# Kernel optimization log

Hardware: AMD Instinct MI355X
Metric: run time of the kernel (lower is better)

Reference implementation:

```python
import jax, jax.numpy as jnp
import numpy as np

H_IMG, W_IMG = 256, 256
FX = FY = 300.0
CX, CY = W_IMG / 2.0, H_IMG / 2.0
NEAR, FAR = 0.01, 100.0
MAX_RADIUS = 64.0
N_GAUSS = 4096


def quat_to_rot(q):
    q = q / jnp.linalg.norm(q, axis=-1, keepdims=True)
    w, x, y, z = q[..., 0], q[..., 1], q[..., 2], q[..., 3]
    R = jnp.stack([
        1 - 2 * y * y - 2 * z * z, 2 * x * y - 2 * w * z, 2 * x * z + 2 * w * y,
        2 * x * y + 2 * w * z, 1 - 2 * x * x - 2 * z * z, 2 * y * z - 2 * w * x,
        2 * x * z - 2 * w * y, 2 * y * z + 2 * w * x, 1 - 2 * x * x - 2 * y * y,
    ], axis=-1)
    return R.reshape(q.shape[:-1] + (3, 3))


def setup_inputs():
    key = jax.random.key(0)
    k1, k2, k3, k4, k5, k6 = jax.random.split(key, 6)
    xy = jax.random.normal(k1, (N_GAUSS, 2), jnp.float32) * 2.0
    z = -(jax.random.uniform(k2, (N_GAUSS, 1), jnp.float32) * 6.0 + 2.0)  # depths in [2, 8]
    positions = jnp.concatenate([xy, z], axis=1)
    scales = jax.random.uniform(k3, (N_GAUSS, 3), jnp.float32) * 0.10 + 0.02
    rotations = jax.random.normal(k4, (N_GAUSS, 4), jnp.float32)
    colors = jax.random.uniform(k5, (N_GAUSS, 3), jnp.float32)
    opacities = jax.random.uniform(k6, (N_GAUSS,), jnp.float32) * 0.8 + 0.1
    view_matrix = jnp.eye(4, dtype=jnp.float32)
    return {"positions": positions, "scales": scales, "rotations": rotations,
            "colors": colors, "opacities": opacities, "view_matrix": view_matrix}


def _render(positions, scales, rotations, colors, opacities, view_matrix):
    N = positions.shape[0]
    pts = jnp.concatenate([positions, jnp.ones((N, 1), positions.dtype)], axis=1)
    pc = (view_matrix @ pts.T).T[:, :3]  # camera-space points (N,3)
    x, y, z = pc[:, 0], pc[:, 1], pc[:, 2]
    depths = -z
    z_safe = jnp.clip(jnp.abs(z), 0.01) * jnp.sign(z + 1e-8)
    z2 = z_safe * z_safe
    # 3D covariance = (Rcam R S)(Rcam R S)^T
    R = quat_to_rot(rotations)
    R_cam = view_matrix[:3, :3] @ R
    RS = R_cam * scales[:, None, :]  # right-multiply by diag(scales)
    cov3d = RS @ jnp.swapaxes(RS, -1, -2)
    # perspective Jacobian (N,2,3)
    zr = jnp.zeros_like(x)
    J = jnp.stack([
        jnp.stack([FX / -z_safe, zr, FX * x / z2], axis=-1),
        jnp.stack([zr, FY / z_safe, FY * y / z2], axis=-1),
    ], axis=-2)
    cov2d = J @ cov3d @ jnp.swapaxes(J, -1, -2)
    u = FX * x / -z_safe + CX
    v = FY * -y / -z_safe + CY
    # effective radius: 3 sigma from max eigenvalue of 2x2 covariance
    a, b = cov2d[:, 0, 0], cov2d[:, 0, 1]
    c, d = cov2d[:, 1, 0], cov2d[:, 1, 1]
    tr = a + d
    det = jnp.clip(a * d - b * c, 1e-6)
    disc = jnp.clip(tr * tr - 4.0 * det, 0.0)
    lam = (tr + jnp.sqrt(disc)) * 0.5
    radii = jnp.minimum(3.0 * jnp.sqrt(jnp.clip(lam, 1e-6)), MAX_RADIUS)
    # depth sort (front to back)
    order = jnp.argsort(depths)
    u, v, a, b, c, d = u[order], v[order], a[order], b[order], c[order], d[order]
    radii, depths = radii[order], depths[order]
    colors_s, op_s = colors[order], opacities[order]
    # visibility culling: zero opacity instead of compaction (same math, static shapes)
    visible = (depths > NEAR) & (depths < FAR)
    visible &= (u + radii > 0) & (u - radii < W_IMG)
    visible &= (v + radii > 0) & (v - radii < H_IMG)
    op_s = jnp.where(visible, op_s, 0.0)
    # regularized 2x2 inverse (pinv of PD matrix == inverse)
    ar, dr = a + 1e-4, d + 1e-4
    inv_det = 1.0 / (ar * dr - b * c)
    ia, ib, ic, idd = dr * inv_det, -b * inv_det, -c * inv_det, ar * inv_det
    px = jnp.arange(W_IMG, dtype=jnp.float32)[None, :]
    py = jnp.arange(H_IMG, dtype=jnp.float32)[:, None]

    def step(carry, g):
        acc_c, acc_a = carry
        mx, my, gia, gib, gic, gid, r, col, o = g
        dx = px - mx  # (1,W)
        dy = py - my  # (H,1)
        power = -0.5 * (gia * dx * dx + (gib + gic) * dx * dy + gid * dy * dy)
        # bounding-box mask replicating the torch tile bounds [int(m-r), int(m+r)+1)
        inside = ((px >= jnp.trunc(mx - r)) & (px <= jnp.trunc(mx + r))
                  & (py >= jnp.trunc(my - r)) & (py <= jnp.trunc(my + r)))
        alpha = jnp.where(inside, o * jnp.exp(power), 0.0)
        w = alpha * (1.0 - acc_a)  # front-to-back over-compositing
        return (acc_c + w[..., None] * col, acc_a + w), None

    acc0 = (jnp.zeros((H_IMG, W_IMG, 3), jnp.float32),
            jnp.zeros((H_IMG, W_IMG), jnp.float32))
    (acc_c, acc_a), _ = jax.lax.scan(
        step, acc0, (u, v, ia, ib, ic, idd, radii, colors_s, op_s))
    bg = jnp.zeros(3, jnp.float32)
    img = acc_c + (1.0 - acc_a)[..., None] * bg
    return jnp.transpose(img, (2, 0, 1))  # (3,H,W)


def reference(positions, scales, rotations, colors, opacities, view_matrix):
    return _render(positions, scales, rotations, colors, opacities, view_matrix)
```

## Files before the change

### kernel.cpp

```cpp
#include <hip/hip_runtime.h>
#include <hip/hip_fp16.h>
#include <math.h>

#define N_G   4096
#define CAP   1024
#define W_IMG 256
#define H_IMG 256

__global__ __launch_bounds__(256) void prep(
    const float* __restrict__ pos, const float* __restrict__ scl,
    const float* __restrict__ rot, const float* __restrict__ col,
    const float* __restrict__ opa, const float* __restrict__ vm,
    float4* __restrict__ gaussU, short4* __restrict__ bbhU,
    float* __restrict__ depthU)
{
  const int i = blockIdx.x * 256 + threadIdx.x;
  if (i >= N_G) return;
  const float FX=300.f, FY=300.f, CXc=128.f, CYc=128.f;
  const float HLOG2E = 0.72134752f;
  float V00=vm[0],V01=vm[1],V02=vm[2],V03=vm[3];
  float V10=vm[4],V11=vm[5],V12=vm[6],V13=vm[7];
  float V20=vm[8],V21=vm[9],V22=vm[10],V23=vm[11];
  float p0=pos[3*i], p1=pos[3*i+1], p2=pos[3*i+2];
  float X = V00*p0+V01*p1+V02*p2+V03;
  float Y = V10*p0+V11*p1+V12*p2+V13;
  float Z = V20*p0+V21*p1+V22*p2+V23;
  float depth = -Z;
  float zp = Z + 1e-8f;
  float sgn = (zp>0.f)?1.f:((zp<0.f)?-1.f:0.f);
  float z_safe = fmaxf(fabsf(Z), 0.01f) * sgn;
  float z2 = z_safe*z_safe;
  float qw=rot[4*i], qx=rot[4*i+1], qy=rot[4*i+2], qz=rot[4*i+3];
  float qi = 1.f/sqrtf(qw*qw+qx*qx+qy*qy+qz*qz);
  qw*=qi; qx*=qi; qy*=qi; qz*=qi;
  float R00=1.f-2.f*qy*qy-2.f*qz*qz, R01=2.f*qx*qy-2.f*qw*qz, R02=2.f*qx*qz+2.f*qw*qy;
  float R10=2.f*qx*qy+2.f*qw*qz, R11=1.f-2.f*qx*qx-2.f*qz*qz, R12=2.f*qy*qz-2.f*qw*qx;
  float R20=2.f*qx*qz-2.f*qw*qy, R21=2.f*qy*qz+2.f*qw*qx, R22=1.f-2.f*qx*qx-2.f*qy*qy;
  float C00=V00*R00+V01*R10+V02*R20, C01=V00*R01+V01*R11+V02*R21, C02=V00*R02+V01*R12+V02*R22;
  float C10=V10*R00+V11*R10+V12*R20, C11=V10*R01+V11*R11+V12*R21, C12=V10*R02+V11*R12+V12*R22;
  float C20=V20*R00+V21*R10+V22*R20, C21=V20*R01+V21*R11+V22*R21, C22=V20*R02+V21*R12+V22*R22;
  float s0=scl[3*i], s1=scl[3*i+1], s2=scl[3*i+2];
  float S00=C00*s0,S01=C01*s1,S02=C02*s2;
  float S10=C10*s0,S11=C11*s1,S12=C12*s2;
  float S20=C20*s0,S21=C21*s1,S22=C22*s2;
  float c00=S00*S00+S01*S01+S02*S02;
  float c01=S00*S10+S01*S11+S02*S12;
  float c02=S00*S20+S01*S21+S02*S22;
  float c11=S10*S10+S11*S11+S12*S12;
  float c12=S10*S20+S11*S21+S12*S22;
  float c22=S20*S20+S21*S21+S22*S22;
  float j00=FX/(-z_safe), j02=FX*X/z2;
  float j11=FY/z_safe,    j12=FY*Y/z2;
  float M00=j00*c00+j02*c02, M01=j00*c01+j02*c12, M02=j00*c02+j02*c22;
  float M10=j11*c01+j12*c02, M11=j11*c11+j12*c12, M12=j11*c12+j12*c22;
  float a =M00*j00+M02*j02;
  float b =M01*j11+M02*j12;
  float c_=M10*j00+M12*j02;
  float d =M11*j11+M12*j12;
  float u = FX*X/(-z_safe)+CXc;
  float v = FY*(-Y)/(-z_safe)+CYc;
  float tr=a+d;
  float det=fmaxf(a*d-b*c_, 1e-6f);
  float disc=fmaxf(tr*tr-4.f*det, 0.f);
  float lam=(tr+sqrtf(disc))*0.5f;
  float radius=fminf(3.f*sqrtf(fmaxf(lam,1e-6f)), 64.f);
  bool vis = (depth>0.01f)&&(depth<100.f)
          && (u+radius>0.f)&&(u-radius<(float)W_IMG)
          && (v+radius>0.f)&&(v-radius<(float)H_IMG);
  float o = vis ? opa[i] : 0.f;
  float ar=a+1e-4f, dr=d+1e-4f;
  float inv=1.f/(ar*dr-b*c_);
  short4 bb = make_short4(1000, -1000, 1000, -1000);
  if (o>0.f) {
    bb.x=(short)truncf(u-radius); bb.y=(short)truncf(u+radius);
    bb.z=(short)truncf(v-radius); bb.w=(short)truncf(v+radius);
  }
  unsigned hrg = (unsigned)__half_as_ushort(__float2half_rn(col[3*i]))
               | ((unsigned)__half_as_ushort(__float2half_rn(col[3*i+1]))<<16);
  depthU[i] = depth;
  bbhU[i]   = bb;
  gaussU[2*i]   = make_float4(u, v, (dr*inv)*HLOG2E,
                              ((-b*inv)+(-c_*inv))*HLOG2E);
  gaussU[2*i+1] = make_float4((ar*inv)*HLOG2E, log2f(o),
                              __uint_as_float(hrg), col[3*i+2]);
}

__global__ __launch_bounds__(1024) void render(
    const short4* __restrict__ bbhU, const float4* __restrict__ gaussU,
    const float* __restrict__ depthU, float* __restrict__ out)
{
  __shared__ __align__(16) unsigned long long keys[CAP+2];
  __shared__ unsigned short sidx[CAP];
  __shared__ float4 gp[CAP*2];
  __shared__ short4 bbh[CAP];
  __shared__ float4 res[16][64];
  __shared__ unsigned long long smsk[64];
  __shared__ int scnt[64], soff[64], slen;

  const int tid = threadIdx.x, wv = tid>>6, lane = tid&63;
  const int bid = (int)((blockIdx.x * 331u) & 511u);
  const int RX0=(bid&15)*16, RY0=(bid>>4)*8;
  const int RX1=RX0+15, RY1=RY0+7;

  {
    short4 bb[4];
    #pragma unroll
    for (int c4=0;c4<4;c4++) bb[c4]=bbhU[(wv*4+c4)*64+lane];
    #pragma unroll
    for (int c4=0;c4<4;c4++) {
      int c=wv*4+c4;
      bool pred=(bb[c4].y>=RX0)&&(bb[c4].x<=RX1)&&(bb[c4].w>=RY0)&&(bb[c4].z<=RY1);
      unsigned long long m=__ballot(pred);
      if(lane==0){ smsk[c]=m; scnt[c]=__popcll(m); }
    }
  }
  __syncthreads();
  if (wv==0) {
    int cc=scnt[lane];
    int x=cc;
    #pragma unroll
    for(int d=1;d<64;d<<=1){ int y=__shfl_up(x,d); if(lane>=d) x+=y; }
    soff[lane]=x-cc;
    if(lane==63) slen=(x<CAP)?x:CAP;
  }
  __syncthreads();
  const int len=slen;
  #pragma unroll
  for (int c4=0;c4<4;c4++) {
    int c=wv*4+c4;
    unsigned long long m=smsk[c];
    int off=soff[c];
    if((m>>lane)&1ull){
      int p=off+__popcll(m&((1ull<<lane)-1ull));
      int idx=c*64+lane;
      if(p<CAP)
        keys[p]=((unsigned long long)__float_as_uint(depthU[idx])<<12)
               |(unsigned)idx;
    }
  }
  if(tid==0){ keys[len]=~0ull; keys[len+1]=~0ull; }
  __syncthreads();

  if(tid<len){
    unsigned long long kj=keys[tid];
    int r=0;
    const ulonglong2* k2=(const ulonglong2*)keys;
    int n2=(len+1)>>1;
    for(int s2=0;s2<n2;s2++){
      ulonglong2 kv=k2[s2];
      r += (kv.x<kj)+(kv.y<kj);
    }
    sidx[r]=(unsigned short)(kj&4095u);
  }
  __syncthreads();
  if(tid<len){
    int idx=(int)sidx[tid];
    gp[2*tid]  =gaussU[2*idx];
    gp[2*tid+1]=gaussU[2*idx+1];
    bbh[tid]   =bbhU[idx];
  }
  __syncthreads();

  const int t=wv>>3, seg=wv&7;
  const int TX0=RX0+t*8, TY0=RY0, TX1=TX0+7, TY1=TY0+7;
  const int ipx=TX0+(lane&7), ipy=TY0+(lane>>3);
  const float px=(float)ipx, py=(float)ipy;
  const int segLen=(len+7)>>3;
  const int s=seg*segLen;
  int e=s+segLen; if(e>len) e=len;
  float aR=0.f,aG=0.f,aB=0.f,aA=0.f;
  for(int k0=s;k0<e;k0+=64){
    int kk=k0+lane;
    bool ok=false;
    if(kk<e){
      short4 bb=bbh[kk];
      ok=(bb.y>=TX0)&&(bb.x<=TX1)&&(bb.w>=TY0)&&(bb.z<=TY1);
    }
    unsigned long long mm=__ballot(ok);
    while(mm){
      int k=k0+__builtin_ctzll(mm); mm&=mm-1;
      short4 bb=bbh[k];
      float4 A=gp[2*k], B=gp[2*k+1];
      float dx=px-A.x, dy=py-A.y;
      float q2=A.z*dx*dx + A.w*dx*dy + B.x*dy*dy;
      bool inside=(ipx>=bb.x)&&(ipx<=bb.y)&&(ipy>=bb.z)&&(ipy<=bb.w);
      float ex=__builtin_amdgcn_exp2f(B.y-q2);
      float alpha= inside ? ex : 0.f;
      float w=alpha*(1.f-aA);
      unsigned hrg=__float_as_uint(B.z);
      float cR=__half2float(__ushort_as_half((unsigned short)(hrg&0xFFFFu)));
      float cG=__half2float(__ushort_as_half((unsigned short)(hrg>>16)));
      aR+=w*cR; aG+=w*cG; aB+=w*B.w; aA+=w;
    }
    if(__ballot(aA<=0.9999f)==0ull) break;
  }
  res[wv][lane]=make_float4(aR,aG,aB,aA);
  __syncthreads();

  if(seg==0){
    float4 P=res[wv][lane];
    #pragma unroll
    for(int w=1;w<8;w++){
      float4 Q=res[wv+w][lane];
      float tr_=1.f-P.w;
      P.x+=tr_*Q.x; P.y+=tr_*Q.y; P.z+=tr_*Q.z; P.w+=tr_*Q.w;
    }
    out[0*H_IMG*W_IMG + ipy*W_IMG + ipx]=P.x;
    out[1*H_IMG*W_IMG + ipy*W_IMG + ipx]=P.y;
    out[2*H_IMG*W_IMG + ipy*W_IMG + ipx]=P.z;
  }
}

extern "C" void kernel_launch(void* const* d_in, const int* in_sizes, int n_in,
                              void* d_out, int out_size, void* d_ws, size_t ws_size,
                              hipStream_t stream)
{
  const float* pos=(const float*)d_in[0];
  const float* scl=(const float*)d_in[1];
  const float* rot=(const float*)d_in[2];
  const float* col=(const float*)d_in[3];
  const float* opa=(const float*)d_in[4];
  const float* vm =(const float*)d_in[5];
  float* out=(float*)d_out;
  char* ws=(char*)d_ws;
  float4* gaussU=(float4*)(ws);
  short4* bbhU  =(short4*)(ws + 128*1024);
  float*  depthU=(float*) (ws + 160*1024);
  prep<<<N_G/256, 256, 0, stream>>>(pos,scl,rot,col,opa,vm,gaussU,bbhU,depthU);
  render<<<512, 1024, 0, stream>>>(bbhU,gaussU,depthU,out);
}
```

Measured before the change: 19.85 us.

## Use atomic compaction, fuse rank-sort scatter with gather, prefetch next gaussian

Replaces the ballot-count plus prefix-scan compaction with a per-wave atomicAdd on a shared counter, removing one barrier and the scan pass. The rank sort now gathers gaussian data directly to its sorted slot, eliminating the sidx array and another barrier. The compositing loop loads the next gaussian's parameters before computing the current one to hide LDS latency. Atomic ordering is nondeterministic, but the depth-index keys keep the final sort deterministic. The sentinel keys are replaced by explicit odd-length handling.

```diff
diff --git a/kernel.cpp b/kernel.cpp
--- a/kernel.cpp
+++ b/kernel.cpp
@@ -89,18 +89,19 @@
     const short4* __restrict__ bbhU, const float4* __restrict__ gaussU,
     const float* __restrict__ depthU, float* __restrict__ out)
 {
-  __shared__ __align__(16) unsigned long long keys[CAP+2];
-  __shared__ unsigned short sidx[CAP];
+  __shared__ __align__(16) unsigned long long keys[CAP];
   __shared__ float4 gp[CAP*2];
   __shared__ short4 bbh[CAP];
   __shared__ float4 res[16][64];
-  __shared__ unsigned long long smsk[64];
-  __shared__ int scnt[64], soff[64], slen;
+  __shared__ int lcnt;
 
   const int tid = threadIdx.x, wv = tid>>6, lane = tid&63;
   const int bid = (int)((blockIdx.x * 331u) & 511u);
   const int RX0=(bid&15)*16, RY0=(bid>>4)*8;
   const int RX1=RX0+15, RY1=RY0+7;
+
+  if (tid==0) lcnt=0;
+  __syncthreads();
 
   {
     short4 bb[4];
@@ -108,56 +109,39 @@
     for (int c4=0;c4<4;c4++) bb[c4]=bbhU[(wv*4+c4)*64+lane];
     #pragma unroll
     for (int c4=0;c4<4;c4++) {
-      int c=wv*4+c4;
+      int idx=(wv*4+c4)*64+lane;
       bool pred=(bb[c4].y>=RX0)&&(bb[c4].x<=RX1)&&(bb[c4].w>=RY0)&&(bb[c4].z<=RY1);
       unsigned long long m=__ballot(pred);
-      if(lane==0){ smsk[c]=m; scnt[c]=__popcll(m); }
-    }
-  }
-  __syncthreads();
-  if (wv==0) {
-    int cc=scnt[lane];
-    int x=cc;
-    #pragma unroll
-    for(int d=1;d<64;d<<=1){ int y=__shfl_up(x,d); if(lane>=d) x+=y; }
-    soff[lane]=x-cc;
-    if(lane==63) slen=(x<CAP)?x:CAP;
-  }
-  __syncthreads();
-  const int len=slen;
-  #pragma unroll
-  for (int c4=0;c4<4;c4++) {
-    int c=wv*4+c4;
-    unsigned long long m=smsk[c];
-    int off=soff[c];
-    if((m>>lane)&1ull){
-      int p=off+__popcll(m&((1ull<<lane)-1ull));
-      int idx=c*64+lane;
-      if(p<CAP)
-        keys[p]=((unsigned long long)__float_as_uint(depthU[idx])<<12)
-               |(unsigned)idx;
-    }
-  }
-  if(tid==0){ keys[len]=~0ull; keys[len+1]=~0ull; }
-  __syncthreads();
-
-  if(tid<len){
+      if (m) {
+        int bse=0;
+        if (lane==0) bse=atomicAdd(&lcnt, __popcll(m));
+        bse=__shfl(bse,0);
+        if (pred) {
+          int p=bse+__popcll(m&((1ull<<lane)-1ull));
+          if (p<CAP)
+            keys[p]=((unsigned long long)__float_as_uint(depthU[idx])<<12)
+                   |(unsigned)idx;
+        }
+      }
+    }
+  }
+  __syncthreads();
+  const int len = (lcnt<CAP)?lcnt:CAP;
+
+  if (tid<len) {
     unsigned long long kj=keys[tid];
     int r=0;
     const ulonglong2* k2=(const ulonglong2*)keys;
-    int n2=(len+1)>>1;
+    int n2=len>>1;
     for(int s2=0;s2<n2;s2++){
       ulonglong2 kv=k2[s2];
       r += (kv.x<kj)+(kv.y<kj);
     }
-    sidx[r]=(unsigned short)(kj&4095u);
-  }
-  __syncthreads();
-  if(tid<len){
-    int idx=(int)sidx[tid];
-    gp[2*tid]  =gaussU[2*idx];
-    gp[2*tid+1]=gaussU[2*idx+1];
-    bbh[tid]   =bbhU[idx];
+    if(len&1) r += (keys[len-1]<kj);
+    int idx=(int)(kj&4095u);
+    gp[2*r]  =gaussU[2*idx];
+    gp[2*r+1]=gaussU[2*idx+1];
+    bbh[r]   =bbhU[idx];
   }
   __syncthreads();
 
@@ -177,10 +161,26 @@
       ok=(bb.y>=TX0)&&(bb.x<=TX1)&&(bb.w>=TY0)&&(bb.z<=TY1);
     }
     unsigned long long mm=__ballot(ok);
-    while(mm){
+    if(mm){
       int k=k0+__builtin_ctzll(mm); mm&=mm-1;
       short4 bb=bbh[k];
       float4 A=gp[2*k], B=gp[2*k+1];
+      while(mm){
+        int kn=k0+__builtin_ctzll(mm); mm&=mm-1;
+        short4 bbn=bbh[kn];
+        float4 An=gp[2*kn], Bn=gp[2*kn+1];
+        float dx=px-A.x, dy=py-A.y;
+        float q2=A.z*dx*dx + A.w*dx*dy + B.x*dy*dy;
+        bool inside=(ipx>=bb.x)&&(ipx<=bb.y)&&(ipy>=bb.z)&&(ipy<=bb.w);
+        float ex=__builtin_amdgcn_exp2f(B.y-q2);
+        float alpha= inside ? ex : 0.f;
+        float w=alpha*(1.f-aA);
+        unsigned hrg=__float_as_uint(B.z);
+        float cR=__half2float(__ushort_as_half((unsigned short)(hrg&0xFFFFu)));
+        float cG=__half2float(__ushort_as_half((unsigned short)(hrg>>16)));
+        aR+=w*cR; aG+=w*cG; aB+=w*B.w; aA+=w;
+        bb=bbn; A=An; B=Bn;
+      }
       float dx=px-A.x, dy=py-A.y;
       float q2=A.z*dx*dx + A.w*dx*dy + B.x*dy*dy;
       bool inside=(ipx>=bb.x)&&(ipx<=bb.y)&&(ipy>=bb.z)&&(ipy<=bb.w);
```

Result: faster. 19.24 us (-3.1%).
